# Performance work log

Hardware: AMD Instinct MI355X
Metric: run time of the kernel (lower is better)

## Reference

```python
import jax, jax.numpy as jnp
import numpy as np

N_NODES = 10000


def _sage_pool(h, src, dst, Wp, bp, Ws, Wn, b):
    # DGL SAGEConv 'pool': m = relu(fc_pool(h_src)); neigh = max over in-edges;
    # out = fc_self(h_dst) + fc_neigh(neigh) + bias. Zero-in-degree nodes get 0 neigh.
    m = jax.nn.relu(h @ Wp + bp)                      # [N, d_in] node-level transform
    neigh = jax.ops.segment_max(m[src], dst, num_segments=N_NODES)  # [N, d_in]
    neigh = jnp.where(jnp.isfinite(neigh), neigh, 0.0)  # empty segments filled -inf -> 0
    return h @ Ws + neigh @ Wn + b


def setup_inputs() -> dict:
    key = jax.random.key(0)
    ks = jax.random.split(key, 20)
    dims = [(960, 512), (512, 512), (512, 1)]
    inp = {
        "h": jax.random.normal(ks[0], (N_NODES, 960), dtype=jnp.float32),
        "src": jax.random.randint(ks[1], (160000,), 0, N_NODES),
        "dst": jax.random.randint(ks[2], (160000,), 0, N_NODES),
    }
    ki = 3
    for l, (di, do) in enumerate(dims):
        inp[f"Wp{l}"] = jax.random.normal(ks[ki + 0], (di, di), dtype=jnp.float32) * 0.02
        inp[f"bp{l}"] = jnp.zeros((di,), dtype=jnp.float32)
        inp[f"Ws{l}"] = jax.random.normal(ks[ki + 1], (di, do), dtype=jnp.float32) * 0.02
        inp[f"Wn{l}"] = jax.random.normal(ks[ki + 2], (di, do), dtype=jnp.float32) * 0.02
        inp[f"b{l}"] = jnp.zeros((do,), dtype=jnp.float32)
        ki += 3
    return inp


def reference(h, src, dst,
              Wp0, bp0, Ws0, Wn0, b0,
              Wp1, bp1, Ws1, Wn1, b1,
              Wp2, bp2, Ws2, Wn2, b2):
    # layer 0: 960 -> 512, relu (dropout = identity in eval)
    x = jax.nn.relu(_sage_pool(h, src, dst, Wp0, bp0, Ws0, Wn0, b0))
    # layer 1: 512 -> 512, relu
    x = jax.nn.relu(_sage_pool(x, src, dst, Wp1, bp1, Ws1, Wn1, b1))
    # layer 2: 512 -> 1, sigmoid, squeeze -> per-node prediction
    x = _sage_pool(x, src, dst, Wp2, bp2, Ws2, Wn2, b2)
    return jax.nn.sigmoid(x).squeeze(-1)  # [N]
```

## Files before the change

### kernel.cpp

```cpp
#include <hip/hip_runtime.h>
#include <stdint.h>

#define NN 10000
#define NE 160000
#define MPAD 10112
#define MTILES 79

typedef unsigned short u16;
typedef float f32x4 __attribute__((ext_vector_type(4)));
typedef short short8 __attribute__((ext_vector_type(8)));
typedef __bf16 bf16x8 __attribute__((ext_vector_type(8)));
typedef unsigned short u16x4 __attribute__((ext_vector_type(4)));
typedef unsigned short u16x8 __attribute__((ext_vector_type(8)));

__device__ __forceinline__ float bf2f(u16 u) {
  union { unsigned u; float f; } c; c.u = ((unsigned)u) << 16; return c.f;
}
__device__ __forceinline__ u16 f2bf(float f) {
  union { float f; unsigned u; } c; c.f = f;
  return (u16)((c.u + 0x7FFFu + ((c.u >> 16) & 1u)) >> 16);
}

__device__ __forceinline__ void gld_lds16(void* lds, const void* g) {
  __builtin_amdgcn_global_load_lds(
      (const unsigned int __attribute__((address_space(1)))*)g,
      (unsigned int __attribute__((address_space(3)))*)lds, 16, 0, 0);
}

__global__ __launch_bounds__(256) void deg_count(const int* __restrict__ dst, int* __restrict__ deg) {
  int e = blockIdx.x * 256 + threadIdx.x;
  if (e < NE) atomicAdd(&deg[dst[e]], 1);
}

__global__ __launch_bounds__(256) void scan_off(const int* __restrict__ deg,
                                                int* __restrict__ roff, int* __restrict__ cur) {
  __shared__ int part[256];
  const int t = threadIdx.x;
  const int CH = 40;
  int s = 0;
  for (int i = 0; i < CH; ++i) { int idx = t * CH + i; if (idx < NN) s += deg[idx]; }
  part[t] = s; __syncthreads();
  for (int off = 1; off < 256; off <<= 1) {
    int v = (t >= off) ? part[t - off] : 0;
    __syncthreads(); part[t] += v; __syncthreads();
  }
  int run = (t == 0) ? 0 : part[t - 1];
  for (int i = 0; i < CH; ++i) {
    int idx = t * CH + i;
    if (idx < NN) { roff[idx] = run; cur[idx] = run; run += deg[idx]; }
  }
  if (t == 255) roff[NN] = NE;
}

__global__ __launch_bounds__(256) void fill_csr(const int* __restrict__ src, const int* __restrict__ dst,
                                                int* __restrict__ cur, int* __restrict__ esrc) {
  int e = blockIdx.x * 256 + threadIdx.x;
  if (e < NE) {
    int p = atomicAdd(&cur[dst[e]], 1);
    esrc[p] = src[e];
  }
}

__global__ __launch_bounds__(256) void convert_h(const float* __restrict__ h, u16* __restrict__ hbf) {
  const size_t i = (size_t)(blockIdx.x * 256 + threadIdx.x) * 4;
  if (i >= (size_t)MPAD * 960) return;
  u16x4 o;
  if (i < (size_t)NN * 960) {
    float4 v = *(const float4*)(h + i);
    o[0] = f2bf(v.x); o[1] = f2bf(v.y); o[2] = f2bf(v.z); o[3] = f2bf(v.w);
  } else {
    o[0] = 0; o[1] = 0; o[2] = 0; o[3] = 0;
  }
  *(u16x4*)(hbf + i) = o;
}

struct WDesc { const float* in; u16* out; int R, C, Cpad, ldo, koff; };
struct WPack { WDesc d[7]; };

__global__ __launch_bounds__(256) void transpose_all(WPack p) {
  const WDesc w = p.d[blockIdx.z];
  const int cb = blockIdx.x * 32, rb = blockIdx.y * 32;
  if (cb >= w.Cpad || rb >= w.R) return;
  __shared__ float tile[32][33];
  const int tx = threadIdx.x & 31, ty = threadIdx.x >> 5;
  for (int i = ty; i < 32; i += 8) {
    int r = rb + i, c = cb + tx;
    tile[i][tx] = (r < w.R && c < w.C) ? w.in[(size_t)r * w.C + c] : 0.f;
  }
  __syncthreads();
  for (int i = ty; i < 32; i += 8) {
    int c = cb + i, r = rb + tx;
    if (c < w.Cpad && r < w.R) w.out[(size_t)c * w.ldo + w.koff + r] = f2bf(tile[tx][i]);
  }
}

template<int TM, int TN, int MINB>
__global__ __launch_bounds__(256, MINB) void gemm3(
    const u16* __restrict__ A0, int lda0,
    const u16* __restrict__ A1, int lda1, int ksplit,
    const u16* __restrict__ B,
    const float* __restrict__ bias, int nbias,
    u16* __restrict__ Cb, int ldcb,
    int K, int act, int tiles_n) {
  constexpr int TR = TM + TN;
  constexpr int NC = TR / 32;
  constexpr int WCOLS = (TM == 128) ? 2 : 4;
  constexpr int WN = TN / WCOLS;
  constexpr int NJ = WN / 16;
  constexpr int MT = MPAD / TM;
  __shared__ __align__(16) u16 S0[TR * 64];
  __shared__ __align__(16) u16 S1[TR * 64];
  const int tid = threadIdx.x;
  const int wave = tid >> 6, lane = tid & 63;

  const int nwg = tiles_n * MT;
  const int orig = blockIdx.x + blockIdx.y * tiles_n;
  const int q = nwg >> 3, r8 = nwg & 7;
  const int xcd = orig & 7, idx = orig >> 3;
  const int wg = (xcd < r8 ? xcd * (q + 1) : r8 * (q + 1) + (xcd - r8) * q) + idx;
  const int tm = (wg / tiles_n) * TM;
  const int tn = (wg % tiles_n) * TN;

  const int wr = (wave / WCOLS) * 64;
  const int wc = (wave % WCOLS) * WN;
  const int fr = lane & 15, fq = lane >> 4;
  const int sr8 = lane >> 3;
  const int sslot = lane & 7;
  f32x4 acc[4][NJ] = {};

  auto stage = [&](u16* Sw, int kk) {
#pragma unroll
    for (int c = 0; c < NC; ++c) {
      const int row = c * 32 + wave * 8 + sr8;
      const int gs = (sslot ^ (row & 7)) * 8;
      const void* g;
      if (c < NC * TM / TR) {
        g = (kk < ksplit)
            ? (const void*)&A0[(size_t)(tm + row) * lda0 + kk + gs]
            : (const void*)&A1[(size_t)(tm + row) * lda1 + (kk - ksplit) + gs];
      } else {
        g = (const void*)&B[(size_t)(tn + row - TM) * (size_t)K + kk + gs];
      }
      gld_lds16(&Sw[(c * 32 + wave * 8) * 64], g);
    }
  };

  const int nsteps = K >> 6;
  stage(S0, 0);
  stage(S1, 64);
  for (int base = 0; base < nsteps; base += 2) {
#pragma unroll
    for (int ph = 0; ph < 2; ++ph) {
      const int t = base + ph;
      if (t >= nsteps) break;
      u16* Sr = (ph == 0) ? S0 : S1;
      if (t + 1 < nsteps) {
        asm volatile("s_waitcnt vmcnt(%0)" :: "i"(NC) : "memory");
      } else {
        asm volatile("s_waitcnt vmcnt(0)" ::: "memory");
      }
      __builtin_amdgcn_s_barrier();
      __builtin_amdgcn_sched_barrier(0);
      short8 af[4][2], bfr[2][NJ];
#pragma unroll
      for (int i = 0; i < 4; ++i) {
        const int r = wr + i * 16 + fr;
#pragma unroll
        for (int kc = 0; kc < 2; ++kc)
          af[i][kc] = *(const short8*)&Sr[r * 64 + ((((kc << 2) | fq) ^ (r & 7)) << 3)];
      }
#pragma unroll
      for (int j = 0; j < NJ; ++j) {
        const int r = TM + wc + j * 16 + fr;
#pragma unroll
        for (int kc = 0; kc < 2; ++kc)
          bfr[kc][j] = *(const short8*)&Sr[r * 64 + ((((kc << 2) | fq) ^ (r & 7)) << 3)];
      }
      asm volatile("s_waitcnt lgkmcnt(0)" ::: "memory");
      __builtin_amdgcn_sched_barrier(0);
      __builtin_amdgcn_s_barrier();
      if (t + 2 < nsteps) stage(Sr, (t + 2) << 6);
      __builtin_amdgcn_s_setprio(1);
#pragma unroll
      for (int kc = 0; kc < 2; ++kc)
#pragma unroll
        for (int i = 0; i < 4; ++i)
#pragma unroll
          for (int j = 0; j < NJ; ++j)
            acc[i][j] = __builtin_amdgcn_mfma_f32_16x16x32_bf16(
                __builtin_bit_cast(bf16x8, af[i][kc]), __builtin_bit_cast(bf16x8, bfr[kc][j]),
                acc[i][j], 0, 0, 0);
      __builtin_amdgcn_s_setprio(0);
      __builtin_amdgcn_sched_barrier(0);
    }
  }

  const int cr = fq * 4, cc = fr;
#pragma unroll
  for (int i = 0; i < 4; ++i)
#pragma unroll
    for (int j = 0; j < NJ; ++j) {
      const int col = tn + wc + j * 16 + cc;
      const float bv = (col < nbias) ? bias[col] : 0.f;
#pragma unroll
      for (int r = 0; r < 4; ++r) {
        const int row = tm + wr + i * 16 + cr + r;
        float v = acc[i][j][r] + bv;
        if (act) v = fmaxf(v, 0.f);
        Cb[(size_t)row * ldcb + col] = f2bf(v);
      }
    }
}

template<int CW>
__global__ __launch_bounds__(256) void aggregate_xcd(
    const u16* __restrict__ m, int ldm, const int* __restrict__ roff,
    const int* __restrict__ esrc, u16* __restrict__ neigh, int ldn) {
  constexpr int TPN = CW / 8;
  constexpr int NPB = 256 / TPN;
  const int chunk = blockIdx.x & 7;
  const int node = (blockIdx.x >> 3) * NPB + threadIdx.x / TPN;
  if (node >= NN) return;
  const int fi = chunk * CW + (threadIdx.x % TPN) * 8;
  const int beg = roff[node], end = roff[node + 1];
  u16x8 a;
#pragma unroll
  for (int i = 0; i < 8; ++i) a[i] = 0;
  for (int e = beg; e < end; ++e) {
    const u16* row = m + (size_t)esrc[e] * ldm;
    u16x8 v = *(const u16x8*)(row + fi);
#pragma unroll
    for (int i = 0; i < 8; ++i) a[i] = (v[i] > a[i]) ? v[i] : a[i];
  }
  *(u16x8*)(neigh + (size_t)node * ldn + fi) = a;
}

__global__ __launch_bounds__(256) void final_out(
    const u16* __restrict__ x, const u16* __restrict__ neigh,
    const float* __restrict__ ws, const float* __restrict__ wn,
    const float* __restrict__ b, float* __restrict__ out) {
  const int wave = threadIdx.x >> 6, lane = threadIdx.x & 63;
  const int n = blockIdx.x * 4 + wave;
  if (n >= NN) return;
  const int f = lane * 8;
  const u16* xr = x + (size_t)n * 512 + f;
  const u16* nr = neigh + (size_t)n * 512 + f;
  float s = 0.f;
#pragma unroll
  for (int i = 0; i < 8; ++i)
    s += bf2f(xr[i]) * ws[f + i] + bf2f(nr[i]) * wn[f + i];
#pragma unroll
  for (int o = 32; o > 0; o >>= 1) s += __shfl_xor(s, o);
  if (lane == 0) out[n] = 1.f / (1.f + expf(-(s + b[0])));
}

extern "C" void kernel_launch(void* const* d_in, const int* in_sizes, int n_in,
                              void* d_out, int out_size, void* d_ws, size_t ws_size,
                              hipStream_t stream) {
  const float* h   = (const float*)d_in[0];
  const int*   src = (const int*)d_in[1];
  const int*   dst = (const int*)d_in[2];
  const float* Wp0 = (const float*)d_in[3];
  const float* bp0 = (const float*)d_in[4];
  const float* Ws0 = (const float*)d_in[5];
  const float* Wn0 = (const float*)d_in[6];
  const float* b0  = (const float*)d_in[7];
  const float* Wp1 = (const float*)d_in[8];
  const float* bp1 = (const float*)d_in[9];
  const float* Ws1 = (const float*)d_in[10];
  const float* Wn1 = (const float*)d_in[11];
  const float* b1  = (const float*)d_in[12];
  const float* Wp2 = (const float*)d_in[13];
  const float* bp2 = (const float*)d_in[14];
  const float* Ws2 = (const float*)d_in[15];
  const float* Wn2 = (const float*)d_in[16];
  const float* b2  = (const float*)d_in[17];
  float* out = (float*)d_out;

  char* ws = (char*)d_ws;
  size_t off = 0;
  auto alloc = [&](size_t n) { char* p = ws + off; off = (off + n + 255) & ~(size_t)255; return p; };
  u16* hbf   = (u16*)alloc((size_t)MPAD * 960 * 2);
  u16* x1    = (u16*)alloc((size_t)MPAD * 512 * 2);
  u16* x2    = (u16*)alloc((size_t)MPAD * 512 * 2);
  u16* mbuf  = (u16*)alloc((size_t)MPAD * 1024 * 2);
  u16* nbuf  = (u16*)alloc((size_t)MPAD * 1024 * 2);
  u16* WpT0  = (u16*)alloc((size_t)1024 * 960 * 2);
  u16* Bcat0 = (u16*)alloc((size_t)512 * 1920 * 2);
  u16* WpT1  = (u16*)alloc((size_t)512 * 512 * 2);
  u16* Bcat1 = (u16*)alloc((size_t)512 * 1024 * 2);
  u16* WpT2  = (u16*)alloc((size_t)512 * 512 * 2);
  int* deg   = (int*)alloc(NN * 4);
  int* roff  = (int*)alloc((NN + 1) * 4);
  int* curp  = (int*)alloc(NN * 4);
  int* esrc  = (int*)alloc(NE * 4);

  hipMemsetAsync(deg, 0, NN * 4, stream);
  deg_count<<<NE / 256, 256, 0, stream>>>(dst, deg);
  scan_off<<<1, 256, 0, stream>>>(deg, roff, curp);
  fill_csr<<<NE / 256, 256, 0, stream>>>(src, dst, curp, esrc);
  convert_h<<<(MPAD * 960 / 4) / 256, 256, 0, stream>>>(h, hbf);

  WPack wp;
  wp.d[0] = {Wp0, WpT0,  960, 960, 1024,  960,   0};
  wp.d[1] = {Ws0, Bcat0, 960, 512,  512, 1920,   0};
  wp.d[2] = {Wn0, Bcat0, 960, 512,  512, 1920, 960};
  wp.d[3] = {Wp1, WpT1,  512, 512,  512,  512,   0};
  wp.d[4] = {Ws1, Bcat1, 512, 512,  512, 1024,   0};
  wp.d[5] = {Wn1, Bcat1, 512, 512,  512, 1024, 512};
  wp.d[6] = {Wp2, WpT2,  512, 512,  512,  512,   0};
  transpose_all<<<dim3(32, 30, 7), 256, 0, stream>>>(wp);

  gemm3<128, 128, 2><<<dim3(8, 79), 256, 0, stream>>>(
      hbf, 960, hbf, 960, 960, WpT0, bp0, 960, mbuf, 1024, 960, 1, 8);
  aggregate_xcd<128><<<5000, 256, 0, stream>>>(mbuf, 1024, roff, esrc, nbuf, 1024);
  gemm3<128, 128, 2><<<dim3(4, 79), 256, 0, stream>>>(
      hbf, 960, nbuf, 1024, 960, Bcat0, b0, 512, x1, 512, 1920, 1, 4);

  gemm3<128, 128, 2><<<dim3(4, 79), 256, 0, stream>>>(
      x1, 512, x1, 512, 512, WpT1, bp1, 512, mbuf, 512, 512, 1, 4);
  aggregate_xcd<64><<<2504, 256, 0, stream>>>(mbuf, 512, roff, esrc, nbuf, 512);
  gemm3<128, 128, 2><<<dim3(4, 79), 256, 0, stream>>>(
      x1, 512, nbuf, 512, 512, Bcat1, b1, 512, x2, 512, 1024, 1, 4);

  gemm3<128, 128, 2><<<dim3(4, 79), 256, 0, stream>>>(
      x2, 512, x2, 512, 512, WpT2, bp2, 512, mbuf, 512, 512, 1, 4);
  aggregate_xcd<64><<<2504, 256, 0, stream>>>(mbuf, 512, roff, esrc, nbuf, 512);
  final_out<<<2500, 256, 0, stream>>>(x2, nbuf, Ws2, Wn2, b2, out);
}
```

Before: 260.5 us.

## Load GEMM B operand straight to registers and triple-buffer A in LDS

```diff
diff --git a/kernel.cpp b/kernel.cpp
--- a/kernel.cpp
+++ b/kernel.cpp
@@ -102,14 +102,14 @@
     const float* __restrict__ bias, int nbias,
     u16* __restrict__ Cb, int ldcb,
     int K, int act, int tiles_n) {
-  constexpr int TR = TM + TN;
-  constexpr int NC = TR / 32;
-  constexpr int WCOLS = (TM == 128) ? 2 : 4;
+  constexpr int NC = TM / 32;
+  constexpr int WCOLS = 2;
   constexpr int WN = TN / WCOLS;
   constexpr int NJ = WN / 16;
   constexpr int MT = MPAD / TM;
-  __shared__ __align__(16) u16 S0[TR * 64];
-  __shared__ __align__(16) u16 S1[TR * 64];
+  __shared__ __align__(16) u16 S0[TM * 64];
+  __shared__ __align__(16) u16 S1[TM * 64];
+  __shared__ __align__(16) u16 S2[TM * 64];
   const int tid = threadIdx.x;
   const int wave = tid >> 6, lane = tid & 63;
 
@@ -133,66 +133,68 @@
     for (int c = 0; c < NC; ++c) {
       const int row = c * 32 + wave * 8 + sr8;
       const int gs = (sslot ^ (row & 7)) * 8;
-      const void* g;
-      if (c < NC * TM / TR) {
-        g = (kk < ksplit)
-            ? (const void*)&A0[(size_t)(tm + row) * lda0 + kk + gs]
-            : (const void*)&A1[(size_t)(tm + row) * lda1 + (kk - ksplit) + gs];
-      } else {
-        g = (const void*)&B[(size_t)(tn + row - TM) * (size_t)K + kk + gs];
-      }
+      const void* g = (kk < ksplit)
+          ? (const void*)&A0[(size_t)(tm + row) * lda0 + kk + gs]
+          : (const void*)&A1[(size_t)(tm + row) * lda1 + (kk - ksplit) + gs];
       gld_lds16(&Sw[(c * 32 + wave * 8) * 64], g);
     }
   };
 
+  auto loadB = [&](short8 (&bf)[2 * NJ], int kk) {
+#pragma unroll
+    for (int j = 0; j < NJ; ++j)
+#pragma unroll
+      for (int kc = 0; kc < 2; ++kc)
+        bf[j * 2 + kc] = *(const short8*)&B[
+            (size_t)(tn + wc + j * 16 + fr) * (size_t)K + kk + (((kc << 2) | fq) << 3)];
+  };
+
   const int nsteps = K >> 6;
+  short8 b0[2 * NJ], b1[2 * NJ], b2[2 * NJ];
+
   stage(S0, 0);
+  loadB(b0, 0);
+  __builtin_amdgcn_sched_barrier(0);
   stage(S1, 64);
-  for (int base = 0; base < nsteps; base += 2) {
-#pragma unroll
-    for (int ph = 0; ph < 2; ++ph) {
-      const int t = base + ph;
-      if (t >= nsteps) break;
-      u16* Sr = (ph == 0) ? S0 : S1;
-      if (t + 1 < nsteps) {
-        asm volatile("s_waitcnt vmcnt(%0)" :: "i"(NC) : "memory");
-      } else {
-        asm volatile("s_waitcnt vmcnt(0)" ::: "memory");
-      }
-      __builtin_amdgcn_s_barrier();
-      __builtin_amdgcn_sched_barrier(0);
-      short8 af[4][2], bfr[2][NJ];
-#pragma unroll
-      for (int i = 0; i < 4; ++i) {
-        const int r = wr + i * 16 + fr;
-#pragma unroll
-        for (int kc = 0; kc < 2; ++kc)
-          af[i][kc] = *(const short8*)&Sr[r * 64 + ((((kc << 2) | fq) ^ (r & 7)) << 3)];
-      }
-#pragma unroll
-      for (int j = 0; j < NJ; ++j) {
-        const int r = TM + wc + j * 16 + fr;
-#pragma unroll
-        for (int kc = 0; kc < 2; ++kc)
-          bfr[kc][j] = *(const short8*)&Sr[r * 64 + ((((kc << 2) | fq) ^ (r & 7)) << 3)];
-      }
-      asm volatile("s_waitcnt lgkmcnt(0)" ::: "memory");
-      __builtin_amdgcn_sched_barrier(0);
-      __builtin_amdgcn_s_barrier();
-      if (t + 2 < nsteps) stage(Sr, (t + 2) << 6);
-      __builtin_amdgcn_s_setprio(1);
+
+  auto phase = [&](int t, const u16* Sr, u16* Sw,
+                   short8 (&bc)[2 * NJ], short8 (&bn)[2 * NJ]) {
+    if (t + 1 < nsteps) {
+      asm volatile("s_waitcnt vmcnt(%0)" :: "i"(NC) : "memory");
+    } else {
+      asm volatile("s_waitcnt vmcnt(0)" ::: "memory");
+    }
+    __builtin_amdgcn_s_barrier();
+    __builtin_amdgcn_sched_barrier(0);
+    short8 af[4][2];
+#pragma unroll
+    for (int i = 0; i < 4; ++i) {
+      const int r = wr + i * 16 + fr;
 #pragma unroll
       for (int kc = 0; kc < 2; ++kc)
-#pragma unroll
-        for (int i = 0; i < 4; ++i)
-#pragma unroll
-          for (int j = 0; j < NJ; ++j)
-            acc[i][j] = __builtin_amdgcn_mfma_f32_16x16x32_bf16(
-                __builtin_bit_cast(bf16x8, af[i][kc]), __builtin_bit_cast(bf16x8, bfr[kc][j]),
-                acc[i][j], 0, 0, 0);
-      __builtin_amdgcn_s_setprio(0);
-      __builtin_amdgcn_sched_barrier(0);
+        af[i][kc] = *(const short8*)&Sr[r * 64 + ((((kc << 2) | fq) ^ (r & 7)) << 3)];
     }
+    if (t + 1 < nsteps) loadB(bn, (t + 1) << 6);
+    __builtin_amdgcn_sched_barrier(0);
+    if (t + 2 < nsteps) stage(Sw, (t + 2) << 6);
+    __builtin_amdgcn_s_setprio(1);
+#pragma unroll
+    for (int kc = 0; kc < 2; ++kc)
+#pragma unroll
+      for (int i = 0; i < 4; ++i)
+#pragma unroll
+        for (int j = 0; j < NJ; ++j)
+          acc[i][j] = __builtin_amdgcn_mfma_f32_16x16x32_bf16(
+              __builtin_bit_cast(bf16x8, af[i][kc]), __builtin_bit_cast(bf16x8, bc[j * 2 + kc]),
+              acc[i][j], 0, 0, 0);
+    __builtin_amdgcn_s_setprio(0);
+    __builtin_amdgcn_sched_barrier(0);
+  };
+
+  for (int base = 0; base < nsteps; base += 3) {
+    phase(base, S0, S2, b0, b1);
+    if (base + 1 < nsteps) phase(base + 1, S1, S0, b1, b2);
+    if (base + 2 < nsteps) phase(base + 2, S2, S1, b2, b0);
   }
 
   const int cr = fq * 4, cc = fr;
```

Result: slower. 362.7 us (+39.2%).
